# Kernel optimization log

Hardware: AMD Instinct MI355X
Metric: run time of the kernel (lower is better)

Reference implementation:

```python
import jax, jax.numpy as jnp
import numpy as np

NEG_SLOPE = 0.2  # PyG GATv2 leaky_relu slope
LN_EPS = 1e-5


def _layernorm(x, gamma, beta):
    mu = x.mean(-1, keepdims=True)
    var = x.var(-1, keepdims=True)
    return (x - mu) * jax.lax.rsqrt(var + LN_EPS) * gamma + beta


def _gatv2_conv(x, src, dst, eattr, Wl, Wr, We, att, bias, concat):
    """PyG GATv2Conv (eval mode). x:(N,F), src/dst:(E,), eattr:(E,edge_dim), att:(H,C)."""
    N = x.shape[0]
    H, C = att.shape
    xl = (x @ Wl).reshape(N, H, C)   # source transform (messages)
    xr = (x @ Wr).reshape(N, H, C)   # target transform
    e = (eattr @ We).reshape(-1, H, C)
    m = xl[src] + xr[dst] + e                                   # (E,H,C)
    score = jnp.sum(jax.nn.leaky_relu(m, NEG_SLOPE) * att, -1)  # (E,H)
    # segment softmax over incoming edges per destination node
    smax = jax.ops.segment_max(score, dst, num_segments=N)
    ex = jnp.exp(score - smax[dst])
    denom = jax.ops.segment_sum(ex, dst, num_segments=N)
    alpha = ex / (denom[dst] + 1e-16)                           # (E,H)
    out = jax.ops.segment_sum(alpha[:, :, None] * xl[src], dst, num_segments=N)  # (N,H,C)
    out = out.reshape(N, H * C) if concat else out.mean(axis=1)
    return out + bias


def setup_inputs() -> dict:
    key = jax.random.key(0)
    ks = jax.random.split(key, 20)
    N, E = 10000, 320000
    D, HID, HEADS, ED = 256, 128, 4, 4
    HC = HID * HEADS  # 512

    def w(k, fi, fo):
        return jax.random.normal(k, (fi, fo), jnp.float32) / np.sqrt(fi)

    x = jax.random.normal(ks[0], (N, D), jnp.float32)
    edge_index = jax.random.randint(ks[1], (2, E), 0, N, jnp.int64)
    edge_attr = jax.random.normal(ks[2], (E, ED), jnp.float32)
    return {
        "x": x, "edge_index": edge_index, "edge_attr": edge_attr,
        # layer 1: heads=4, concat=True
        "Wl1": w(ks[3], D, HC), "Wr1": w(ks[4], D, HC), "We1": w(ks[5], ED, HC),
        "att1": jax.random.normal(ks[6], (HEADS, HID), jnp.float32) / np.sqrt(HID),
        "b1": jnp.zeros((HC,), jnp.float32),
        "g1": jnp.ones((HC,), jnp.float32), "be1": jnp.zeros((HC,), jnp.float32),
        # layer 2: heads=1, concat=False
        "Wl2": w(ks[7], HC, D), "Wr2": w(ks[8], HC, D), "We2": w(ks[9], ED, D),
        "att2": jax.random.normal(ks[10], (1, D), jnp.float32) / np.sqrt(D),
        "b2": jnp.zeros((D,), jnp.float32),
        "g2": jnp.ones((D,), jnp.float32), "be2": jnp.zeros((D,), jnp.float32),
    }


def reference(x, edge_index, edge_attr,
              Wl1, Wr1, We1, att1, b1, g1, be1,
              Wl2, Wr2, We2, att2, b2, g2, be2):
    N = x.shape[0]
    # PyG default add_self_loops=True with edge_attr fill_value='mean'
    loop = jnp.arange(N, dtype=edge_index.dtype)
    src = jnp.concatenate([edge_index[0], loop])
    dst = jnp.concatenate([edge_index[1], loop])
    ea = jnp.concatenate([edge_attr, jnp.broadcast_to(edge_attr.mean(0), (N, edge_attr.shape[1]))])

    h = _gatv2_conv(x, src, dst, ea, Wl1, Wr1, We1, att1, b1, concat=True)
    h = _layernorm(h, g1, be1)
    h = jax.nn.elu(h)  # dropout is identity in eval mode

    h = _gatv2_conv(h, src, dst, ea, Wl2, Wr2, We2, att2, b2, concat=False)
    h = _layernorm(h, g2, be2)
    return h + x  # residual (in_channels == out_channels)
```

## Files before the change

### kernel.cpp

```cpp
#include <hip/hip_runtime.h>
#include <hip/hip_bf16.h>

#define HC1 512
#define HC2 256
#define D_IN 256

typedef __hip_bfloat16  bf16;
typedef __hip_bfloat162 bf162;
typedef __attribute__((ext_vector_type(8))) short short8;
typedef __attribute__((ext_vector_type(4))) float f32x4;
typedef __attribute__((ext_vector_type(2))) float f32x2;

__device__ __forceinline__ void unpack8p(short8 q, f32x2* xa) {
  union { short8 s; unsigned u[4]; } uu; uu.s = q;
#pragma unroll
  for (int j = 0; j < 4; j++) {
    union { unsigned u; float f; } lo, hi;
    lo.u = uu.u[j] << 16;
    hi.u = uu.u[j] & 0xffff0000u;
    xa[j].x = lo.f; xa[j].y = hi.f;
  }
}
__device__ __forceinline__ void unpack4p(short4 qs, f32x2* xa) {
  union { short4 s; unsigned u[2]; } uu; uu.s = qs;
#pragma unroll
  for (int j = 0; j < 2; j++) {
    union { unsigned u; float f; } lo, hi;
    lo.u = uu.u[j] << 16;
    hi.u = uu.u[j] & 0xffff0000u;
    xa[j].x = lo.f; xa[j].y = hi.f;
  }
}
__device__ __forceinline__ void load8p(const float* p, f32x2* d) {
  float4 a = *(const float4*)p, b = *(const float4*)(p + 4);
  d[0].x = a.x; d[0].y = a.y; d[1].x = a.z; d[1].y = a.w;
  d[2].x = b.x; d[2].y = b.y; d[3].x = b.z; d[3].y = b.w;
}
__device__ __forceinline__ void load4p(const float* p, f32x2* d) {
  float4 a = *(const float4*)p;
  d[0].x = a.x; d[0].y = a.y; d[1].x = a.z; d[1].y = a.w;
}

template <int CTRL>
__device__ __forceinline__ float dppadd(float x) {
  union { float f; int i; } u, v;
  u.f = x;
  v.i = __builtin_amdgcn_update_dpp(0, u.i, CTRL, 0xF, 0xF, true);
  return x + v.f;
}
__device__ __forceinline__ float red16(float p) {
  p = dppadd<0xB1>(p);
  p = dppadd<0x4E>(p);
  p = dppadd<0x124>(p);
  p = dppadd<0x128>(p);
  return p;
}

__device__ __forceinline__ void glds16(const bf16* g, bf16* l) {
#if __has_builtin(__builtin_amdgcn_global_load_lds)
  __builtin_amdgcn_global_load_lds(
      (const __attribute__((address_space(1))) void*)g,
      (__attribute__((address_space(3))) void*)l, 16, 0, 0);
#else
  int lane = threadIdx.x & 63;
  ((int4*)l)[lane] = *(const int4*)g;
#endif
}

__global__ __launch_bounds__(256)
void gemm_mfma_kernel(const bf16* __restrict__ A, const bf16* __restrict__ BT,
                      bf16* __restrict__ C, int M, int K, int N) {
  __shared__ bf16 lds[8192];
  const int t = threadIdx.x;
  const int w  = t >> 6, l = t & 63;
  const int wr = w >> 1, wc = w & 1;
  const int lo = l & 15, hi = l >> 4;
  const int m0 = blockIdx.y * 128;
  const int n0 = blockIdx.x * 128;

  f32x4 acc[4][4] = {};

  const int c0 = w * 2, c1 = w * 2 + 1;
  const int kc0 = c0 >> 1, r0 = (c0 & 1) * 64 + l;
  const int kc1 = c1 >> 1, r1 = (c1 & 1) * 64 + l;
  int mr0 = m0 + r0; if (mr0 >= M) mr0 = M - 1;
  int mr1 = m0 + r1; if (mr1 >= M) mr1 = M - 1;
  const bf16* ga0 = A + (size_t)mr0 * K + kc0 * 8;
  const bf16* ga1 = A + (size_t)mr1 * K + kc1 * 8;
  const bf16* gb0 = BT + (size_t)(n0 + r0) * K + kc0 * 8;
  const bf16* gb1 = BT + (size_t)(n0 + r1) * K + kc1 * 8;
  bf16* la0 = &lds[c0 * 512];
  bf16* la1 = &lds[c1 * 512];
  bf16* lb0 = &lds[4096 + c0 * 512];
  bf16* lb1 = &lds[4096 + c1 * 512];

  for (int k0 = 0; k0 < K; k0 += 32) {
    if (k0) __syncthreads();
    glds16(ga0 + k0, la0);
    glds16(ga1 + k0, la1);
    glds16(gb0 + k0, lb0);
    glds16(gb1 + k0, lb1);
    __syncthreads();

    short8 af[4], bfr[4];
#pragma unroll
    for (int f = 0; f < 4; f++) {
      af[f]  = *(const short8*)&lds[hi * 1024 + (wr * 64 + f * 16 + lo) * 8];
      bfr[f] = *(const short8*)&lds[4096 + hi * 1024 + (wc * 64 + f * 16 + lo) * 8];
    }
#pragma unroll
    for (int fm = 0; fm < 4; fm++)
#pragma unroll
      for (int fn = 0; fn < 4; fn++)
        acc[fm][fn] = __builtin_amdgcn_mfma_f32_16x16x32_bf16(af[fm], bfr[fn],
                                                              acc[fm][fn], 0, 0, 0);
  }

#pragma unroll
  for (int fm = 0; fm < 4; fm++) {
#pragma unroll
    for (int r = 0; r < 4; r++) {
      int row = m0 + wr * 64 + fm * 16 + hi * 4 + r;
      if (row < M) {
#pragma unroll
        for (int fn = 0; fn < 4; fn++) {
          int col = n0 + wc * 64 + fn * 16 + lo;
          C[(size_t)row * N + col] = __float2bfloat16(acc[fm][fn][r]);
        }
      }
    }
  }
}

__global__ void convx_kernel(const float* __restrict__ x, bf16* __restrict__ xb, int n4) {
  int i = blockIdx.x * blockDim.x + threadIdx.x;
  if (i >= n4) return;
  float4 v = ((const float4*)x)[i];
  union { bf16 h[4]; uint2 u; } cv;
  cv.h[0] = __float2bfloat16(v.x); cv.h[1] = __float2bfloat16(v.y);
  cv.h[2] = __float2bfloat16(v.z); cv.h[3] = __float2bfloat16(v.w);
  ((uint2*)xb)[i] = cv.u;
}

__global__ __launch_bounds__(256)
void transw_kernel(const float* __restrict__ Wl1, const float* __restrict__ Wr1,
                   const float* __restrict__ Wl2, const float* __restrict__ Wr2,
                   bf16* __restrict__ W1T, bf16* __restrict__ W2T) {
  __shared__ float tile[32][33];
  const int z = blockIdx.z;
  const float* in; bf16* out; int K, Nn;
  if (z == 0)      { in = Wl1; out = W1T;             K = 256; Nn = 512; }
  else if (z == 1) { in = Wr1; out = W1T + 512 * 256; K = 256; Nn = 512; }
  else if (z == 2) { in = Wl2; out = W2T;             K = 512; Nn = 256; }
  else             { in = Wr2; out = W2T + 256 * 512; K = 512; Nn = 256; }
  const int nt = blockIdx.x * 32, kt = blockIdx.y * 32;
  if (nt >= Nn || kt >= K) return;
  const int tx = threadIdx.x & 31, ty = threadIdx.x >> 5;
#pragma unroll
  for (int j = 0; j < 4; j++)
    tile[ty + j * 8][tx] = in[(size_t)(kt + ty + j * 8) * Nn + nt + tx];
  __syncthreads();
#pragma unroll
  for (int j = 0; j < 4; j++)
    out[(size_t)(nt + ty + j * 8) * K + kt + tx] = __float2bfloat16(tile[tx][ty + j * 8]);
}

__global__ void mean_kernel(const float* __restrict__ eattr, float* __restrict__ sums, int E) {
  int tid = blockIdx.x * blockDim.x + threadIdx.x;
  int stride = gridDim.x * blockDim.x;
  float l0 = 0.f, l1 = 0.f, l2 = 0.f, l3 = 0.f;
  for (int e = tid; e < E; e += stride) {
    float4 v = ((const float4*)eattr)[e];
    l0 += v.x; l1 += v.y; l2 += v.z; l3 += v.w;
  }
#pragma unroll
  for (int o = 1; o < 64; o <<= 1) {
    l0 += __shfl_xor(l0, o); l1 += __shfl_xor(l1, o);
    l2 += __shfl_xor(l2, o); l3 += __shfl_xor(l3, o);
  }
  if ((threadIdx.x & 63) == 0) {
    atomicAdd(&sums[0], l0); atomicAdd(&sums[1], l1);
    atomicAdd(&sums[2], l2); atomicAdd(&sums[3], l3);
  }
}

__global__ void meanw_kernel(const float* __restrict__ sums, float* __restrict__ mean4, float invE) {
  int t = threadIdx.x;
  if (t < 4) mean4[t] = sums[t] * invE;
}

__global__ void count_kernel(const int* __restrict__ ei, int* __restrict__ counts, int E, int Etot) {
  int tid = blockIdx.x * blockDim.x + threadIdx.x;
  int stride = gridDim.x * blockDim.x;
  for (int e = tid; e < Etot; e += stride) {
    int dst = (e < E) ? ei[E + e] : (e - E);
    atomicAdd(&counts[dst], 1);
  }
}

__global__ __launch_bounds__(1024)
void scan_kernel(const int* __restrict__ counts, int* __restrict__ offs, int N) {
  __shared__ int wsum[16];
  int tid = threadIdx.x, wid = tid >> 6, lane = tid & 63;
  if (tid == 0) offs[0] = 0;
  int carry = 0;
  for (int base = 0; base < N; base += 1024) {
    int i = base + tid;
    int v = (i < N) ? counts[i] : 0;
    int s = v;
#pragma unroll
    for (int o = 1; o < 64; o <<= 1) {
      int u = __shfl_up(s, o);
      if (lane >= o) s += u;
    }
    if (lane == 63) wsum[wid] = s;
    __syncthreads();
    if (wid == 0) {
      int t2 = (lane < 16) ? wsum[lane] : 0;
#pragma unroll
      for (int o = 1; o < 16; o <<= 1) {
        int u = __shfl_up(t2, o);
        if (lane >= o) t2 += u;
      }
      if (lane < 16) wsum[lane] = t2;
    }
    __syncthreads();
    int pre = (wid > 0) ? wsum[wid - 1] : 0;
    int tot = wsum[15];
    if (i < N) offs[i + 1] = carry + pre + s;
    carry += tot;
    __syncthreads();
  }
}

__global__ void fill_kernel(const int* __restrict__ ei, const int* __restrict__ offs,
                            int* __restrict__ cursor, const float* __restrict__ eattr,
                            const float* __restrict__ mean4, int* __restrict__ srcs,
                            float4* __restrict__ eaC, int E, int Etot) {
  int tid = blockIdx.x * blockDim.x + threadIdx.x;
  int stride = gridDim.x * blockDim.x;
  for (int e = tid; e < Etot; e += stride) {
    int src, dst;
    if (e < E) { src = ei[e]; dst = ei[E + e]; } else { src = e - E; dst = src; }
    int pos = atomicAdd(&cursor[dst], 1);
    int slot = offs[dst] + pos;
    srcs[slot] = src;
    eaC[slot] = (e < E) ? ((const float4*)eattr)[e] : *(const float4*)mean4;
  }
}

__global__ __launch_bounds__(256, 4)
void fused1_kernel(const int* __restrict__ srcs, const float4* __restrict__ eaC,
                   const int* __restrict__ offs, const bf16* __restrict__ xlr,
                   const float* __restrict__ We, const float* __restrict__ att,
                   const float* __restrict__ bias, const float* __restrict__ g,
                   const float* __restrict__ be, bf16* __restrict__ h1) {
  const int v = blockIdx.x;
  const int tid = threadIdx.x;
  const int wave = tid >> 6, lane = tid & 63;
  const int ch = lane * 8;

  f32x2 w0p[4], w1p[4], w2p[4], w3p[4], awp[4], xrp[4];
  load8p(We + 0 * HC1 + ch, w0p);
  load8p(We + 1 * HC1 + ch, w1p);
  load8p(We + 2 * HC1 + ch, w2p);
  load8p(We + 3 * HC1 + ch, w3p);
  load8p(att + ch, awp);
  unpack8p(*(const short8*)(xlr + (size_t)v * 1024 + 512 + ch), xrp);

  const int beg = offs[v], end = offs[v + 1];
  const int len = end - beg;
  const int chunk = (len + 3) >> 2;
  int ib = beg + wave * chunk;
  int ie = ib + chunk;
  if (ib > end) ib = end;
  if (ie > end) ie = end;

  float den = 0.f;
  f32x2 accp[4] = {};

  auto edge = [&](short8 q, float4 e) {
    f32x2 xa[4]; unpack8p(q, xa);
    f32x2 p2 = {0.f, 0.f};
#pragma unroll
    for (int j = 0; j < 4; j++) {
      f32x2 m = xa[j] + xrp[j];
      m += e.x * w0p[j];
      m += e.y * w1p[j];
      m += e.z * w2p[j];
      m += e.w * w3p[j];
      f32x2 lm = __builtin_elementwise_max(m, m * 0.2f);
      p2 += lm * awp[j];
    }
    float p = p2.x + p2.y;
    p = red16(p);
    float ex = __expf(p);
    den += ex;
#pragma unroll
    for (int j = 0; j < 4; j++) accp[j] += xa[j] * ex;
  };

  int i = ib;
  if (i + 4 <= ie) {
    int s0 = srcs[i], s1 = srcs[i + 1], s2 = srcs[i + 2], s3 = srcs[i + 3];
    float4 e0 = eaC[i], e1 = eaC[i + 1], e2 = eaC[i + 2], e3 = eaC[i + 3];
    short8 q0 = *(const short8*)(xlr + (size_t)s0 * 1024 + ch);
    short8 q1 = *(const short8*)(xlr + (size_t)s1 * 1024 + ch);
    short8 q2 = *(const short8*)(xlr + (size_t)s2 * 1024 + ch);
    short8 q3 = *(const short8*)(xlr + (size_t)s3 * 1024 + ch);
    i += 4;
    for (; i + 4 <= ie; i += 4) {
      int t0 = srcs[i], t1 = srcs[i + 1], t2 = srcs[i + 2], t3 = srcs[i + 3];
      short8 r0 = *(const short8*)(xlr + (size_t)t0 * 1024 + ch);
      short8 r1 = *(const short8*)(xlr + (size_t)t1 * 1024 + ch);
      short8 r2 = *(const short8*)(xlr + (size_t)t2 * 1024 + ch);
      short8 r3 = *(const short8*)(xlr + (size_t)t3 * 1024 + ch);
      edge(q0, e0); edge(q1, e1); edge(q2, e2); edge(q3, e3);
      e0 = eaC[i]; e1 = eaC[i + 1]; e2 = eaC[i + 2]; e3 = eaC[i + 3];
      q0 = r0; q1 = r1; q2 = r2; q3 = r3;
    }
    edge(q0, e0); edge(q1, e1); edge(q2, e2); edge(q3, e3);
  }
  for (; i < ie; ++i) {
    int s0 = srcs[i];
    float4 e0 = eaC[i];
    short8 q0 = *(const short8*)(xlr + (size_t)s0 * 1024 + ch);
    edge(q0, e0);
  }

  __shared__ float accs[4][HC1];
  __shared__ float dens[4][4];
  __shared__ float2 red[4];
  *(float4*)&accs[wave][ch]     = *(float4*)&accp[0];
  *(float4*)&accs[wave][ch + 4] = *(float4*)&accp[2];
  if ((lane & 15) == 0) dens[wave][lane >> 4] = den;
  __syncthreads();

  const int c = tid * 2;
  const int head = c >> 7;
  const float dtot = dens[0][head] + dens[1][head] + dens[2][head] + dens[3][head];
  const float rden = 1.f / (dtot + 1e-16f);
  float2 a0 = *(float2*)&accs[0][c];
  float2 a1 = *(float2*)&accs[1][c];
  float2 a2 = *(float2*)&accs[2][c];
  float2 a3 = *(float2*)&accs[3][c];
  float2 bv = *(const float2*)(bias + c);
  float val0 = (a0.x + a1.x + a2.x + a3.x) * rden + bv.x;
  float val1 = (a0.y + a1.y + a2.y + a3.y) * rden + bv.y;

  float s1 = val0 + val1, s2 = val0 * val0 + val1 * val1;
  s1 = red16(s1); s2 = red16(s2);
  s1 += __shfl_xor(s1, 16); s2 += __shfl_xor(s2, 16);
  s1 += __shfl_xor(s1, 32); s2 += __shfl_xor(s2, 32);
  if (lane == 0) red[wave] = make_float2(s1, s2);
  __syncthreads();
  float ts1 = red[0].x + red[1].x + red[2].x + red[3].x;
  float ts2 = red[0].y + red[1].y + red[2].y + red[3].y;
  float mu  = ts1 * (1.f / HC1);
  float var = ts2 * (1.f / HC1) - mu * mu;
  float rs  = rsqrtf(var + 1e-5f);

  float2 gv = *(const float2*)(g + c);
  float2 ev = *(const float2*)(be + c);
  float ya = (val0 - mu) * rs * gv.x + ev.x;
  float yb = (val1 - mu) * rs * gv.y + ev.y;
  ya = (ya > 0.f) ? ya : expm1f(ya);
  yb = (yb > 0.f) ? yb : expm1f(yb);
  bf162 hv;
  hv.x = __float2bfloat16(ya); hv.y = __float2bfloat16(yb);
  *(bf162*)(h1 + (size_t)v * HC1 + c) = hv;
}

__global__ __launch_bounds__(256, 4)
void fused2_kernel(const int* __restrict__ srcs, const float4* __restrict__ eaC,
                   const int* __restrict__ offs, const bf16* __restrict__ xlr,
                   const float* __restrict__ We, const float* __restrict__ att,
                   const float* __restrict__ bias, const float* __restrict__ g,
                   const float* __restrict__ be, const float* __restrict__ xin,
                   float* __restrict__ out) {
  const int v = blockIdx.x;
  const int tid = threadIdx.x;
  const int wave = tid >> 6, lane = tid & 63;
  const int c0 = lane * 4;

  f32x2 w0p[2], w1p[2], w2p[2], w3p[2], atp[2], xrp[2];
  load4p(We + 0 * HC2 + c0, w0p);
  load4p(We + 1 * HC2 + c0, w1p);
  load4p(We + 2 * HC2 + c0, w2p);
  load4p(We + 3 * HC2 + c0, w3p);
  load4p(att + c0, atp);
  unpack4p(*(const short4*)(xlr + (size_t)v * 512 + 256 + c0), xrp);

  const int beg = offs[v], end = offs[v + 1];
  const int len = end - beg;
  const int chunk = (len + 3) >> 2;
  int ib = beg + wave * chunk;
  int ie = ib + chunk;
  if (ib > end) ib = end;
  if (ie > end) ie = end;

  float den = 0.f;
  f32x2 accp[2] = {};

  auto edge = [&](short4 qs, float4 e) {
    f32x2 xa[2]; unpack4p(qs, xa);
    f32x2 p2 = {0.f, 0.f};
#pragma unroll
    for (int j = 0; j < 2; j++) {
      f32x2 m = xa[j] + xrp[j];
      m += e.x * w0p[j];
      m += e.y * w1p[j];
      m += e.z * w2p[j];
      m += e.w * w3p[j];
      f32x2 lm = __builtin_elementwise_max(m, m * 0.2f);
      p2 += lm * atp[j];
    }
    float p = p2.x + p2.y;
    p = red16(p);
    p += __shfl_xor(p, 16);
    p += __shfl_xor(p, 32);
    float ex = __expf(p);
    den += ex;
    accp[0] += xa[0] * ex;
    accp[1] += xa[1] * ex;
  };

  int i = ib;
  if (i + 4 <= ie) {
    int s0 = srcs[i], s1 = srcs[i + 1], s2 = srcs[i + 2], s3 = srcs[i + 3];
    float4 e0 = eaC[i], e1 = eaC[i + 1], e2 = eaC[i + 2], e3 = eaC[i + 3];
    short4 q0 = *(const short4*)(xlr + (size_t)s0 * 512 + c0);
    short4 q1 = *(const short4*)(xlr + (size_t)s1 * 512 + c0);
    short4 q2 = *(const short4*)(xlr + (size_t)s2 * 512 + c0);
    short4 q3 = *(const short4*)(xlr + (size_t)s3 * 512 + c0);
    i += 4;
    for (; i + 4 <= ie; i += 4) {
      int t0 = srcs[i], t1 = srcs[i + 1], t2 = srcs[i + 2], t3 = srcs[i + 3];
      short4 r0 = *(const short4*)(xlr + (size_t)t0 * 512 + c0);
      short4 r1 = *(const short4*)(xlr + (size_t)t1 * 512 + c0);
      short4 r2 = *(const short4*)(xlr + (size_t)t2 * 512 + c0);
      short4 r3 = *(const short4*)(xlr + (size_t)t3 * 512 + c0);
      edge(q0, e0); edge(q1, e1); edge(q2, e2); edge(q3, e3);
      e0 = eaC[i]; e1 = eaC[i + 1]; e2 = eaC[i + 2]; e3 = eaC[i + 3];
      q0 = r0; q1 = r1; q2 = r2; q3 = r3;
    }
    edge(q0, e0); edge(q1, e1); edge(q2, e2); edge(q3, e3);
  }
  for (; i < ie; ++i) {
    int s0 = srcs[i];
    float4 e0 = eaC[i];
    short4 q0 = *(const short4*)(xlr + (size_t)s0 * 512 + c0);
    edge(q0, e0);
  }

  __shared__ float accs[4][HC2];
  __shared__ float dens[4];
  __shared__ float2 red[4];
  *(float4*)&accs[wave][c0] = *(float4*)&accp[0];
  if (lane == 0) dens[wave] = den;
  __syncthreads();

  const int c = tid;
  const float dtot = dens[0] + dens[1] + dens[2] + dens[3];
  const float rden = 1.f / (dtot + 1e-16f);
  float val = (accs[0][c] + accs[1][c] + accs[2][c] + accs[3][c]) * rden + bias[c];

  float s1 = val, s2 = val * val;
  s1 = red16(s1); s2 = red16(s2);
  s1 += __shfl_xor(s1, 16); s2 += __shfl_xor(s2, 16);
  s1 += __shfl_xor(s1, 32); s2 += __shfl_xor(s2, 32);
  if (lane == 0) red[wave] = make_float2(s1, s2);
  __syncthreads();
  float ts1 = red[0].x + red[1].x + red[2].x + red[3].x;
  float ts2 = red[0].y + red[1].y + red[2].y + red[3].y;
  float mu  = ts1 * (1.f / HC2);
  float var = ts2 * (1.f / HC2) - mu * mu;
  float rs  = rsqrtf(var + 1e-5f);
  float y = (val - mu) * rs * g[c] + be[c];
  out[(size_t)v * HC2 + c] = y + xin[(size_t)v * HC2 + c];
}

extern "C" void kernel_launch(void* const* d_in, const int* in_sizes, int n_in,
                              void* d_out, int out_size, void* d_ws, size_t ws_size,
                              hipStream_t stream) {
  const float* x     = (const float*)d_in[0];
  const int*   ei    = (const int*)d_in[1];
  const float* eattr = (const float*)d_in[2];
  const float* Wl1   = (const float*)d_in[3];
  const float* Wr1   = (const float*)d_in[4];
  const float* We1   = (const float*)d_in[5];
  const float* att1  = (const float*)d_in[6];
  const float* b1    = (const float*)d_in[7];
  const float* g1    = (const float*)d_in[8];
  const float* be1   = (const float*)d_in[9];
  const float* Wl2   = (const float*)d_in[10];
  const float* Wr2   = (const float*)d_in[11];
  const float* We2   = (const float*)d_in[12];
  const float* att2  = (const float*)d_in[13];
  const float* b2    = (const float*)d_in[14];
  const float* g2    = (const float*)d_in[15];
  const float* be2   = (const float*)d_in[16];

  const int N    = in_sizes[0] / D_IN;
  const int E    = in_sizes[2] / 4;
  const int Etot = E + N;

  char* w = (char*)d_ws;
  auto alloc = [&](size_t bytes) -> void* {
    void* p = (void*)w;
    w += (bytes + 255) & ~(size_t)255;
    return p;
  };
  bf16*   xb    = (bf16*)alloc((size_t)N * D_IN * 2);
  bf16*   W1T   = (bf16*)alloc((size_t)1024 * 256 * 2);
  bf16*   W2T   = (bf16*)alloc((size_t)512 * 512 * 2);
  bf16*   xlr1  = (bf16*)alloc((size_t)N * 1024 * 2);
  bf16*   h1    = (bf16*)alloc((size_t)N * HC1 * 2);
  bf16*   xlr2  = (bf16*)alloc((size_t)N * 512 * 2);
  int*    srcs  = (int*)alloc((size_t)Etot * 4);
  float4* eaC   = (float4*)alloc((size_t)Etot * 16);
  int*    offs  = (int*)alloc((size_t)(N + 1) * 4);
  float*  mean4 = (float*)alloc(64);
  char*   zb    = w;
  int*    counts = (int*)alloc((size_t)N * 4);
  int*    cursor = (int*)alloc((size_t)N * 4);
  float*  sums   = (float*)alloc(64);
  size_t  zbytes = (size_t)(w - zb);

  hipMemsetAsync(zb, 0, zbytes, stream);

  int n4 = N * D_IN / 4;
  convx_kernel<<<(n4 + 255) / 256, 256, 0, stream>>>(x, xb, n4);
  transw_kernel<<<dim3(16, 16, 4), 256, 0, stream>>>(Wl1, Wr1, Wl2, Wr2, W1T, W2T);

  mean_kernel<<<256, 256, 0, stream>>>(eattr, sums, E);
  meanw_kernel<<<1, 64, 0, stream>>>(sums, mean4, 1.f / (float)E);

  count_kernel<<<1024, 256, 0, stream>>>(ei, counts, E, Etot);
  scan_kernel<<<1, 1024, 0, stream>>>(counts, offs, N);
  fill_kernel<<<1024, 256, 0, stream>>>(ei, offs, cursor, eattr, mean4, srcs, eaC, E, Etot);

  dim3 gg1(1024 / 128, (N + 127) / 128);
  gemm_mfma_kernel<<<gg1, 256, 0, stream>>>(xb, W1T, xlr1, N, 256, 1024);

  fused1_kernel<<<N, 256, 0, stream>>>(srcs, eaC, offs, xlr1, We1, att1, b1, g1, be1, h1);

  dim3 gg2(512 / 128, (N + 127) / 128);
  gemm_mfma_kernel<<<gg2, 256, 0, stream>>>(h1, W2T, xlr2, N, 512, 512);

  fused2_kernel<<<N, 256, 0, stream>>>(srcs, eaC, offs, xlr2, We2, att2,
                                       b2, g2, be2, x, (float*)d_out);
}
```

Before: 285.7 us.

## Process two edges per wave in layer-2 aggregation using half-wave 8-channel lanes

In the second GAT layer kernel, each wave now splits into two 32-lane halves, each handling a different edge with 8 channels per lane and 16-byte gathers, instead of one edge per wave with 4 channels per lane. This halves the cross-lane reduction depth per edge and widens the gather loads, with the two halves' accumulators combined by a shuffle at the end. Odd tail edges are masked via a validity flag. Launch bounds for both fused kernels are relaxed from 4 to 3 blocks per CU, which gives the compiler more registers at the cost of occupancy.

```diff
diff --git a/kernel.cpp b/kernel.cpp
--- a/kernel.cpp
+++ b/kernel.cpp
@@ -21,24 +21,10 @@
     xa[j].x = lo.f; xa[j].y = hi.f;
   }
 }
-__device__ __forceinline__ void unpack4p(short4 qs, f32x2* xa) {
-  union { short4 s; unsigned u[2]; } uu; uu.s = qs;
-#pragma unroll
-  for (int j = 0; j < 2; j++) {
-    union { unsigned u; float f; } lo, hi;
-    lo.u = uu.u[j] << 16;
-    hi.u = uu.u[j] & 0xffff0000u;
-    xa[j].x = lo.f; xa[j].y = hi.f;
-  }
-}
 __device__ __forceinline__ void load8p(const float* p, f32x2* d) {
   float4 a = *(const float4*)p, b = *(const float4*)(p + 4);
   d[0].x = a.x; d[0].y = a.y; d[1].x = a.z; d[1].y = a.w;
   d[2].x = b.x; d[2].y = b.y; d[3].x = b.z; d[3].y = b.w;
-}
-__device__ __forceinline__ void load4p(const float* p, f32x2* d) {
-  float4 a = *(const float4*)p;
-  d[0].x = a.x; d[0].y = a.y; d[1].x = a.z; d[1].y = a.w;
 }
 
 template <int CTRL>
@@ -249,7 +235,7 @@
   }
 }
 
-__global__ __launch_bounds__(256, 4)
+__global__ __launch_bounds__(256, 3)
 void fused1_kernel(const int* __restrict__ srcs, const float4* __restrict__ eaC,
                    const int* __restrict__ offs, const bf16* __restrict__ xlr,
                    const float* __restrict__ We, const float* __restrict__ att,
@@ -371,7 +357,7 @@
   *(bf162*)(h1 + (size_t)v * HC1 + c) = hv;
 }
 
-__global__ __launch_bounds__(256, 4)
+__global__ __launch_bounds__(256, 3)
 void fused2_kernel(const int* __restrict__ srcs, const float4* __restrict__ eaC,
                    const int* __restrict__ offs, const bf16* __restrict__ xlr,
                    const float* __restrict__ We, const float* __restrict__ att,
@@ -381,15 +367,17 @@
   const int v = blockIdx.x;
   const int tid = threadIdx.x;
   const int wave = tid >> 6, lane = tid & 63;
-  const int c0 = lane * 4;
-
-  f32x2 w0p[2], w1p[2], w2p[2], w3p[2], atp[2], xrp[2];
-  load4p(We + 0 * HC2 + c0, w0p);
-  load4p(We + 1 * HC2 + c0, w1p);
-  load4p(We + 2 * HC2 + c0, w2p);
-  load4p(We + 3 * HC2 + c0, w3p);
-  load4p(att + c0, atp);
-  unpack4p(*(const short4*)(xlr + (size_t)v * 512 + 256 + c0), xrp);
+  const int half = lane >> 5;
+  const int hl = lane & 31;
+  const int c0 = hl * 8;
+
+  f32x2 w0p[4], w1p[4], w2p[4], w3p[4], atp[4], xrp[4];
+  load8p(We + 0 * HC2 + c0, w0p);
+  load8p(We + 1 * HC2 + c0, w1p);
+  load8p(We + 2 * HC2 + c0, w2p);
+  load8p(We + 3 * HC2 + c0, w3p);
+  load8p(att + c0, atp);
+  unpack8p(*(const short8*)(xlr + (size_t)v * 512 + 256 + c0), xrp);
 
   const int beg = offs[v], end = offs[v + 1];
   const int len = end - beg;
@@ -400,13 +388,13 @@
   if (ie > end) ie = end;
 
   float den = 0.f;
-  f32x2 accp[2] = {};
-
-  auto edge = [&](short4 qs, float4 e) {
-    f32x2 xa[2]; unpack4p(qs, xa);
+  f32x2 accp[4] = {};
+
+  auto pair = [&](short8 q, float4 e, bool bvalid) {
+    f32x2 xa[4]; unpack8p(q, xa);
     f32x2 p2 = {0.f, 0.f};
 #pragma unroll
-    for (int j = 0; j < 2; j++) {
+    for (int j = 0; j < 4; j++) {
       f32x2 m = xa[j] + xrp[j];
       m += e.x * w0p[j];
       m += e.y * w1p[j];
@@ -418,45 +406,53 @@
     float p = p2.x + p2.y;
     p = red16(p);
     p += __shfl_xor(p, 16);
-    p += __shfl_xor(p, 32);
     float ex = __expf(p);
+    if (half && !bvalid) ex = 0.f;
     den += ex;
-    accp[0] += xa[0] * ex;
-    accp[1] += xa[1] * ex;
+#pragma unroll
+    for (int j = 0; j < 4; j++) accp[j] += xa[j] * ex;
   };
 
   int i = ib;
   if (i + 4 <= ie) {
-    int s0 = srcs[i], s1 = srcs[i + 1], s2 = srcs[i + 2], s3 = srcs[i + 3];
-    float4 e0 = eaC[i], e1 = eaC[i + 1], e2 = eaC[i + 2], e3 = eaC[i + 3];
-    short4 q0 = *(const short4*)(xlr + (size_t)s0 * 512 + c0);
-    short4 q1 = *(const short4*)(xlr + (size_t)s1 * 512 + c0);
-    short4 q2 = *(const short4*)(xlr + (size_t)s2 * 512 + c0);
-    short4 q3 = *(const short4*)(xlr + (size_t)s3 * 512 + c0);
+    int sA = srcs[i + half],     sB = srcs[i + 2 + half];
+    float4 eA = eaC[i + half],   eB = eaC[i + 2 + half];
+    short8 qA = *(const short8*)(xlr + (size_t)sA * 512 + c0);
+    short8 qB = *(const short8*)(xlr + (size_t)sB * 512 + c0);
     i += 4;
     for (; i + 4 <= ie; i += 4) {
-      int t0 = srcs[i], t1 = srcs[i + 1], t2 = srcs[i + 2], t3 = srcs[i + 3];
-      short4 r0 = *(const short4*)(xlr + (size_t)t0 * 512 + c0);
-      short4 r1 = *(const short4*)(xlr + (size_t)t1 * 512 + c0);
-      short4 r2 = *(const short4*)(xlr + (size_t)t2 * 512 + c0);
-      short4 r3 = *(const short4*)(xlr + (size_t)t3 * 512 + c0);
-      edge(q0, e0); edge(q1, e1); edge(q2, e2); edge(q3, e3);
-      e0 = eaC[i]; e1 = eaC[i + 1]; e2 = eaC[i + 2]; e3 = eaC[i + 3];
-      q0 = r0; q1 = r1; q2 = r2; q3 = r3;
-    }
-    edge(q0, e0); edge(q1, e1); edge(q2, e2); edge(q3, e3);
-  }
-  for (; i < ie; ++i) {
-    int s0 = srcs[i];
-    float4 e0 = eaC[i];
-    short4 q0 = *(const short4*)(xlr + (size_t)s0 * 512 + c0);
-    edge(q0, e0);
-  }
+      int tA = srcs[i + half], tB = srcs[i + 2 + half];
+      short8 rA = *(const short8*)(xlr + (size_t)tA * 512 + c0);
+      short8 rB = *(const short8*)(xlr + (size_t)tB * 512 + c0);
+      pair(qA, eA, true); pair(qB, eB, true);
+      eA = eaC[i + half]; eB = eaC[i + 2 + half];
+      qA = rA; qB = rB;
+    }
+    pair(qA, eA, true); pair(qB, eB, true);
+  }
+  for (; i < ie; i += 2) {
+    bool hasB = (i + 1 < ie);
+    int idx = i + half; if (idx > ie - 1) idx = i;
+    int s = srcs[idx];
+    float4 e = eaC[idx];
+    short8 q = *(const short8*)(xlr + (size_t)s * 512 + c0);
+    pair(q, e, hasB);
+  }
+
+#pragma unroll
+  for (int j = 0; j < 4; j++) {
+    accp[j].x += __shfl_xor(accp[j].x, 32);
+    accp[j].y += __shfl_xor(accp[j].y, 32);
+  }
+  den += __shfl_xor(den, 32);
 
   __shared__ float accs[4][HC2];
   __shared__ float dens[4];
   __shared__ float2 red[4];
-  *(float4*)&accs[wave][c0] = *(float4*)&accp[0];
+  if (half == 0) {
+    *(float4*)&accs[wave][c0]     = *(float4*)&accp[0];
+    *(float4*)&accs[wave][c0 + 4] = *(float4*)&accp[2];
+  }
   if (lane == 0) dens[wave] = den;
   __syncthreads();
 
```

New measurement: 287.9 us. No clear change (+0.8%).
